# Kernel optimization log

Measured on AMD Instinct MI355X. Metric: run time of the kernel, lower is better.

## Reference

```python
import jax, jax.numpy as jnp
import numpy as np

D_MODEL = 512
HIDDEN = 2 * D_MODEL
B, L = 8, 2048
R_MIN, R_MAX = 0.8, 0.99
LN_EPS = 1e-5


def setup_inputs() -> dict:
    key = jax.random.key(0)
    ks = jax.random.split(key, 12)
    x = jax.random.normal(ks[0], (B, L, D_MODEL), jnp.float32)
    mask = jnp.ones((B, L), jnp.float32)
    # LRU eigenvalue init, exactly as the torch __init__
    u1 = jax.random.uniform(ks[1], (HIDDEN,), jnp.float32)
    u2 = jax.random.uniform(ks[2], (HIDDEN,), jnp.float32)
    nu_log = jnp.log(-0.5 * jnp.log(u1 * (R_MAX ** 2 - R_MIN ** 2) + R_MIN ** 2))
    theta_log = jnp.log(u2 * 2.0 * np.pi)
    diag_lambda = jnp.exp(jax.lax.complex(-jnp.exp(nu_log), jnp.exp(theta_log)))
    gamma_log = jnp.log(jnp.sqrt(1.0 - jnp.abs(diag_lambda) ** 2))
    params_log = jnp.stack([nu_log, theta_log, gamma_log])  # (3, HIDDEN)
    s_in = 1.0 / np.sqrt(D_MODEL)
    s_out = 1.0 / np.sqrt(HIDDEN)
    # complex Linear weights (real+imag parts; trained weights are fully complex)
    W_in_re = jax.random.uniform(ks[3], (HIDDEN, D_MODEL), jnp.float32, -s_in, s_in)
    W_in_im = jax.random.uniform(ks[4], (HIDDEN, D_MODEL), jnp.float32, -s_in, s_in)
    b_in_re = jax.random.uniform(ks[5], (HIDDEN,), jnp.float32, -s_in, s_in)
    b_in_im = jax.random.uniform(ks[6], (HIDDEN,), jnp.float32, -s_in, s_in)
    W_out_re = jax.random.uniform(ks[7], (D_MODEL, HIDDEN), jnp.float32, -s_out, s_out)
    W_out_im = jax.random.uniform(ks[8], (D_MODEL, HIDDEN), jnp.float32, -s_out, s_out)
    b_out_re = jax.random.uniform(ks[9], (D_MODEL,), jnp.float32, -s_out, s_out)
    b_out_im = jax.random.uniform(ks[10], (D_MODEL,), jnp.float32, -s_out, s_out)
    ln_w = jnp.ones((D_MODEL,), jnp.float32)
    ln_b = jnp.zeros((D_MODEL,), jnp.float32)
    return dict(x=x, mask=mask, params_log=params_log,
                W_in_re=W_in_re, W_in_im=W_in_im, b_in_re=b_in_re, b_in_im=b_in_im,
                W_out_re=W_out_re, W_out_im=W_out_im, b_out_re=b_out_re, b_out_im=b_out_im,
                ln_w=ln_w, ln_b=ln_b)


def _lru_parallel_scan(h, lamb, mask, Bn, Ln, Dn):
    # log-depth doubling trick over complex diagonal recurrence (faithful port)
    log2_L = int(np.ceil(np.log2(Ln)))
    for i in range(1, log2_L + 1):
        l = 2 ** i
        h = h.reshape(Bn * Ln // l, l, Dn)
        m = mask.reshape(Bn * Ln // l, l)
        h1, h2 = h[:, : l // 2], h[:, l // 2 :]
        if i > 1:
            lamb = jnp.concatenate([lamb, lamb * lamb[-1]], axis=0)  # powers lam^1..lam^(l/2)
        h2 = h2 + lamb * h1[:, -1:] * m[:, l // 2 - 1 : l // 2, None]
        h = jnp.concatenate([h1, h2], axis=1)
    return h.reshape(Bn, Ln, Dn)


def reference(x, mask, params_log, W_in_re, W_in_im, b_in_re, b_in_im,
              W_out_re, W_out_im, b_out_re, b_out_im, ln_w, ln_b):
    nu, theta, gamma = jnp.exp(params_log)  # each (HIDDEN,)
    lamb = jnp.exp(jax.lax.complex(-nu, theta))[None, :]  # (1, HIDDEN)
    W_in = jax.lax.complex(W_in_re, W_in_im)
    b_in = jax.lax.complex(b_in_re, b_in_im)
    W_out = jax.lax.complex(W_out_re, W_out_im)
    b_out = jax.lax.complex(b_out_re, b_out_im)
    xc = x.astype(jnp.complex64)
    h = (jnp.einsum('bld,hd->blh', xc, W_in) + b_in) * gamma  # (B, L, HIDDEN) complex64
    Bn, Ln, Dn = h.shape
    h = _lru_parallel_scan(h, lamb, mask, Bn, Ln, Dn)
    y = (jnp.einsum('blh,dh->bld', h, W_out) + b_out).real + x  # dropout = identity (eval)
    mean = jnp.mean(y, axis=-1, keepdims=True)
    var = jnp.var(y, axis=-1, keepdims=True)
    return (y - mean) / jnp.sqrt(var + LN_EPS) * ln_w + ln_b
```

## Files before the change

### kernel.cpp

```cpp
#include <hip/hip_runtime.h>
#include <hip/hip_bf16.h>
#include <cstdint>
#include <cstddef>


typedef unsigned short u16;
typedef __attribute__((ext_vector_type(8))) short bf16x8;
typedef __attribute__((ext_vector_type(4))) float f32x4;

#define B_    8
#define L_    2048
#define D_    512
#define H_    1024
#define M_    (B_ * L_)
#define SEG_  64
#define T_    (L_ / SEG_)

__device__ __forceinline__ float b2f(u16 u) {
  union { unsigned int i; float f; } v; v.i = ((unsigned int)u) << 16; return v.f;
}
__device__ __forceinline__ u16 f2b(float f) {
  union { float f; unsigned int i; } v; v.f = f;
  unsigned int x = v.i;
  return (u16)((x + 0x7fffu + ((x >> 16) & 1u)) >> 16);
}

__device__ __forceinline__ void gl2lds16(const void* g, void* l) {
  __builtin_amdgcn_global_load_lds(
      (const __attribute__((address_space(1))) void*)g,
      (__attribute__((address_space(3))) void*)l, 16, 0, 0);
}

__device__ __forceinline__ int ksw8(int row, int c) {
  return (c ^ (row & 7)) & 7;
}

__global__ __launch_bounds__(256) void prep_all(
    const float* __restrict__ x, u16* __restrict__ xb,
    const float* __restrict__ wire, const float* __restrict__ wiim,
    const float* __restrict__ wore, const float* __restrict__ woim,
    const float* __restrict__ bire, const float* __restrict__ biim,
    const float* __restrict__ params,
    u16* __restrict__ winb, u16* __restrict__ wcat, float* __restrict__ bb)
{
  int i = blockIdx.x * 256 + threadIdx.x;
#pragma unroll
  for (int j = 0; j < 4; ++j) {
    int gi = i + j * 524288;
    float4 v = ((const float4*)x)[gi];
    ushort4 o;
    o.x = f2b(v.x); o.y = f2b(v.y); o.z = f2b(v.z); o.w = f2b(v.w);
    ((ushort4*)xb)[gi] = o;
  }
  {
    int cp = i >> 9, k = i & 511;
    float g = expf(params[2 * H_ + cp]);
    winb[(size_t)(2 * cp) * 512 + k]     = f2b(wire[i] * g);
    winb[(size_t)(2 * cp + 1) * 512 + k] = f2b(wiim[i] * g);
  }
  {
    int d = i >> 10, c = i & 1023;
    wcat[(size_t)d * 2048 + 2 * c]     = f2b(wore[i]);
    wcat[(size_t)d * 2048 + 2 * c + 1] = f2b(-woim[i]);
  }
  if (i < 1024) {
    float gb = expf(params[2 * H_ + i]);
    bb[2 * i]     = bire[i] * gb;
    bb[2 * i + 1] = biim[i] * gb;
  }
}

__global__ __launch_bounds__(256, 4) void gemm_scan(
    const u16* __restrict__ A, const u16* __restrict__ Bp,
    const float* __restrict__ mask, const float* __restrict__ params,
    u16* __restrict__ h, const float* __restrict__ bb,
    float2* __restrict__ segfin, float* __restrict__ prodm)
{
  __shared__ __align__(16) u16 sAB[16384];
  __shared__ float mf[128];
  const int K = 512;

  const int tid  = threadIdx.x;
  const int lane = tid & 63;
  const int wave = tid >> 6;
  const int wm = wave >> 1, wn = wave & 1;
  const int m0 = blockIdx.x * 128;
  const int n0 = blockIdx.y * 128;
  const int b  = m0 >> 11;
  const int local0 = m0 & (L_ - 1);

  f32x4 acc[4][4];
#pragma unroll
  for (int i = 0; i < 4; ++i)
#pragma unroll
    for (int j = 0; j < 4; ++j) { f32x4 z = {0.f, 0.f, 0.f, 0.f}; acc[i][j] = z; }

  const int q = lane >> 4;
  const int r = lane & 15;

  for (int k0 = 0; k0 < K; k0 += 64) {
#pragma unroll
    for (int it = 0; it < 4; ++it) {
      int ci  = it * 256 + tid;
      int row = ci >> 3;
      int kc  = ksw8(row, ci & 7);
      gl2lds16(A  + (size_t)(m0 + row) * K + k0 + kc * 8, &sAB[ci * 8]);
      gl2lds16(Bp + (size_t)(n0 + row) * K + k0 + kc * 8, &sAB[8192 + ci * 8]);
    }
    __syncthreads();
#pragma unroll
    for (int kk = 0; kk < 2; ++kk) {
      const int cs = kk * 4 + q;
      bf16x8 af[4], bfv[4];
#pragma unroll
      for (int mt = 0; mt < 4; ++mt) {
        int arow = wm * 64 + mt * 16 + r;
        af[mt] = *(const bf16x8*)&sAB[(arow * 8 + ksw8(arow, cs)) * 8];
      }
#pragma unroll
      for (int nt = 0; nt < 4; ++nt) {
        int brow = wn * 64 + nt * 16 + r;
        bfv[nt] = *(const bf16x8*)&sAB[8192 + (brow * 8 + ksw8(brow, cs)) * 8];
      }
#pragma unroll
      for (int mt = 0; mt < 4; ++mt)
#pragma unroll
        for (int nt = 0; nt < 4; ++nt)
          acc[mt][nt] = __builtin_amdgcn_mfma_f32_16x16x32_bf16(
              bfv[nt], af[mt], acc[mt][nt], 0, 0, 0);
    }
    __syncthreads();
  }

  u16* sH = sAB;
  if (tid < 128)
    mf[tid] = (local0 + tid == 0) ? 0.f
                                  : mask[b * L_ + local0 + tid - 1];
#pragma unroll
  for (int mt = 0; mt < 4; ++mt) {
    const int trow = wm * 64 + mt * 16 + r;
    const int sw = (trow & 7) << 4;
#pragma unroll
    for (int nt = 0; nt < 4; ++nt) {
      const int nc = wn * 64 + nt * 16 + q * 4;
      const float4 b4 = *(const float4*)&bb[n0 + nc];
      ushort4 o;
      o.x = f2b(acc[mt][nt][0] + b4.x);
      o.y = f2b(acc[mt][nt][1] + b4.y);
      o.z = f2b(acc[mt][nt][2] + b4.z);
      o.w = f2b(acc[mt][nt][3] + b4.w);
      *(ushort4*)&sH[trow * 128 + (nc ^ sw)] = o;
    }
  }
  __syncthreads();

#pragma unroll
  for (int it = 0; it < 8; ++it) {
    int flat = it * 256 + tid;
    int row  = flat >> 4;
    int c16  = (flat & 15) * 8;
    bf16x8 v = *(const bf16x8*)&sH[row * 128 + (c16 ^ ((row & 7) << 4))];
    *(bf16x8*)&h[(size_t)(m0 + row) * 2048 + n0 + c16] = v;
  }

  {
    const int sIdx = wave;
    const int cpG  = (n0 >> 1) + lane;
    float nu = expf(params[cpG]);
    float th = expf(params[H_ + cpG]);
    float mg = expf(-nu);
    float lr = mg * cosf(th), li = mg * sinf(th);
    float sr = 0.f, si = 0.f, pm = 1.f;
    const int rbase = sIdx * 32;
#pragma unroll
    for (int t = 0; t < 32; ++t) {
      int row = rbase + t;
      int pos = row * 128 + ((lane * 2) ^ ((row & 7) << 4));
      ushort2 v = *(const ushort2*)&sH[pos];
      float fac = mf[row];
      pm *= fac;
      float nr = b2f(v.x) + fac * (lr * sr - li * si);
      float ni = b2f(v.y) + fac * (lr * si + li * sr);
      sr = nr; si = ni;
    }
    const int sG = (local0 >> 5) + sIdx;
    segfin[(size_t)(b * SEG_ + sG) * H_ + cpG] = make_float2(sr, si);
    if (lane == 0 && n0 == 0) prodm[b * SEG_ + sG] = pm;
  }
}

__global__ __launch_bounds__(256) void scan_carry(
    const float2* __restrict__ segfin, const float* __restrict__ prodm,
    const float* __restrict__ params, float2* __restrict__ carries)
{
  int idx = blockIdx.x * 256 + threadIdx.x;
  int b = idx >> 10, cp = idx & 1023;
  float nu = expf(params[cp]);
  float th = expf(params[H_ + cp]);
  float mg = expf(-nu);
  float ltr = mg * cosf(th), lti = mg * sinf(th);
#pragma unroll
  for (int sq = 0; sq < 5; ++sq) {
    float nr = ltr * ltr - lti * lti;
    float ni = 2.f * ltr * lti;
    ltr = nr; lti = ni;
  }
  float cr = 0.f, ci = 0.f;
  float2 fin = segfin[(size_t)(b * SEG_) * H_ + cp];
  float pmv = prodm[b * SEG_];
  for (int s = 0; s < SEG_; ++s) {
    size_t o = (size_t)(b * SEG_ + s) * H_ + cp;
    carries[o] = make_float2(cr, ci);
    float2 finn; float pmn;
    if (s + 1 < SEG_) { finn = segfin[o + H_]; pmn = prodm[b * SEG_ + s + 1]; }
    float nr = fin.x + pmv * (ltr * cr - lti * ci);
    float ni = fin.y + pmv * (ltr * ci + lti * cr);
    cr = nr; ci = ni;
    fin = finn; pmv = pmn;
  }
}

__global__ __launch_bounds__(256) void scan_full(
    u16* __restrict__ h, const float* __restrict__ mask,
    const float* __restrict__ params, const float2* __restrict__ carries)
{
  const int s = blockIdx.x, b = blockIdx.y;
  const int pa = threadIdx.x * 4;
  float lr[4], li[4], sr[4], si[4];
#pragma unroll
  for (int j = 0; j < 4; ++j) {
    int cp = pa + j;
    float nu = expf(params[cp]);
    float th = expf(params[H_ + cp]);
    float mg = expf(-nu);
    lr[j] = mg * cosf(th);
    li[j] = mg * sinf(th);
    float2 cv = carries[(size_t)(b * SEG_ + s) * H_ + cp];
    sr[j] = cv.x; si[j] = cv.y;
  }
  const int t0 = s * T_;
  u16* p = h + (size_t)(b * L_ + t0) * 2048 + pa * 2;
  const float* mp = mask + b * L_ + t0;
  float fac0;
  if (t0 == 0) fac0 = 0.f; else fac0 = mask[b * L_ + t0 - 1];

  bf16x8 buf[2][8];
#pragma unroll
  for (int j = 0; j < 8; ++j)
    buf[0][j] = *(const bf16x8*)(p + (size_t)j * 2048);
#pragma unroll
  for (int ch = 0; ch < T_ / 8; ++ch) {
    const int cur = ch & 1, nxt = cur ^ 1;
    if (ch < T_ / 8 - 1) {
      u16* pn = p + (size_t)(ch + 1) * 8 * 2048;
#pragma unroll
      for (int j = 0; j < 8; ++j)
        buf[nxt][j] = *(const bf16x8*)(pn + (size_t)j * 2048);
    }
#pragma unroll
    for (int j = 0; j < 8; ++j) {
      int i = ch * 8 + j;
      float fac = (i == 0) ? fac0 : mp[i - 1];
      u16 vv[8], ov[8];
      *(bf16x8*)vv = buf[cur][j];
#pragma unroll
      for (int k = 0; k < 4; ++k) {
        float ar = fac * sr[k], ai = fac * si[k];
        float nr = b2f(vv[2 * k])     + lr[k] * ar - li[k] * ai;
        float ni = b2f(vv[2 * k + 1]) + lr[k] * ai + li[k] * ar;
        sr[k] = nr; si[k] = ni;
        ov[2 * k]     = f2b(nr);
        ov[2 * k + 1] = f2b(ni);
      }
      *(bf16x8*)(p + (size_t)i * 2048) = *(bf16x8*)ov;
    }
  }
}

__global__ __launch_bounds__(512, 2) void gemm2_ln(
    const u16* __restrict__ A, const u16* __restrict__ Bp,
    const float* __restrict__ xg, const float* __restrict__ p0,
    const float* __restrict__ lnw, const float* __restrict__ lnb,
    float* __restrict__ out)
{
  __shared__ __align__(16) u16 smem[2][36864];

  const int K = 2048;
  const int tid  = threadIdx.x;
  const int lane = tid & 63;
  const int wave = tid >> 6;
  const int m0 = blockIdx.x * 64;
  const int q = lane >> 4;
  const int r = lane & 15;

  f32x4 acc[4][4];
#pragma unroll
  for (int i = 0; i < 4; ++i)
#pragma unroll
    for (int j = 0; j < 4; ++j) { f32x4 z = {0.f, 0.f, 0.f, 0.f}; acc[i][j] = z; }

  auto stage = [&](int bsel, int k0) {
    u16* sA = &smem[bsel][0];
    u16* sB = &smem[bsel][4096];
    {
      int ci  = tid;
      int row = ci >> 3;
      int kc  = ksw8(row, ci & 7);
      gl2lds16(A + (size_t)(m0 + row) * K + k0 + kc * 8, sA + ci * 8);
    }
#pragma unroll
    for (int it = 0; it < 8; ++it) {
      int ci  = it * 512 + tid;
      int row = ci >> 3;
      int kc  = ksw8(row, ci & 7);
      gl2lds16(Bp + (size_t)row * K + k0 + kc * 8, sB + ci * 8);
    }
  };

#define WAIT_VM9  asm volatile("s_waitcnt vmcnt(9)"  ::: "memory"); \
                  __builtin_amdgcn_sched_barrier(0)
#define WAIT_VM0  asm volatile("s_waitcnt vmcnt(0)"  ::: "memory"); \
                  __builtin_amdgcn_sched_barrier(0)
#define WAIT_LGKM asm volatile("s_waitcnt lgkmcnt(0)" ::: "memory"); \
                  __builtin_amdgcn_sched_barrier(0)
#define BAR()     __builtin_amdgcn_s_barrier(); \
                  __builtin_amdgcn_sched_barrier(0)

  stage(0, 0);
  stage(1, 64);
  WAIT_VM9;
  BAR();

  for (int t = 0; t < 32; ++t) {
    const int c = t & 1;
    const u16* sA = &smem[c][0];
    const u16* sB = &smem[c][4096];

    bf16x8 af[2][4], bfv[2][4];
#pragma unroll
    for (int kk = 0; kk < 2; ++kk) {
      const int cs = kk * 4 + q;
#pragma unroll
      for (int mt = 0; mt < 4; ++mt) {
        int arow = mt * 16 + r;
        af[kk][mt] = *(const bf16x8*)&sA[(arow * 8 + ksw8(arow, cs)) * 8];
      }
#pragma unroll
      for (int nt = 0; nt < 4; ++nt) {
        int brow = wave * 64 + nt * 16 + r;
        bfv[kk][nt] = *(const bf16x8*)&sB[(brow * 8 + ksw8(brow, cs)) * 8];
      }
    }
    WAIT_LGKM;
    BAR();

    if (t < 30) stage(c, (t + 2) * 64);
    __builtin_amdgcn_sched_barrier(0);

#pragma unroll
    for (int kk = 0; kk < 2; ++kk)
#pragma unroll
      for (int mt = 0; mt < 4; ++mt)
#pragma unroll
        for (int nt = 0; nt < 4; ++nt)
          acc[mt][nt] = __builtin_amdgcn_mfma_f32_16x16x32_bf16(
              bfv[kk][nt], af[kk][mt], acc[mt][nt], 0, 0, 0);

    if (t < 30)      { WAIT_VM9; }
    else if (t == 30){ WAIT_VM0; }
    if (t < 31)      { BAR(); }
  }

#undef WAIT_VM9
#undef WAIT_VM0
#undef WAIT_LGKM
#undef BAR

  __syncthreads();
  float* red_s  = (float*)&smem[0][0];
  float* red_ss = red_s + 512;

  float s[4] = {0.f, 0.f, 0.f, 0.f}, ss[4] = {0.f, 0.f, 0.f, 0.f};
#pragma unroll
  for (int mt = 0; mt < 4; ++mt) {
    const size_t grow = (size_t)(m0 + mt * 16 + r);
#pragma unroll
    for (int nt = 0; nt < 4; ++nt) {
      const int c4 = wave * 64 + nt * 16 + q * 4;
      const float4 b4 = *(const float4*)&p0[c4];
      const float4 x4 = *(const float4*)&xg[grow * 512 + c4];
      acc[mt][nt][0] += b4.x + x4.x;
      acc[mt][nt][1] += b4.y + x4.y;
      acc[mt][nt][2] += b4.z + x4.z;
      acc[mt][nt][3] += b4.w + x4.w;
#pragma unroll
      for (int j = 0; j < 4; ++j) {
        float z = acc[mt][nt][j];
        s[mt] += z; ss[mt] += z * z;
      }
    }
  }
#pragma unroll
  for (int mt = 0; mt < 4; ++mt) {
    s[mt]  += __shfl_xor(s[mt], 16);  s[mt]  += __shfl_xor(s[mt], 32);
    ss[mt] += __shfl_xor(ss[mt], 16); ss[mt] += __shfl_xor(ss[mt], 32);
  }
  if (q == 0) {
#pragma unroll
    for (int mt = 0; mt < 4; ++mt) {
      const int lr_ = mt * 16 + r;
      red_s[wave * 64 + lr_]  = s[mt];
      red_ss[wave * 64 + lr_] = ss[mt];
    }
  }
  __syncthreads();
#pragma unroll
  for (int mt = 0; mt < 4; ++mt) {
    const int lr_ = mt * 16 + r;
    float S = 0.f, SS = 0.f;
#pragma unroll
    for (int w = 0; w < 8; ++w) {
      S  += red_s[w * 64 + lr_];
      SS += red_ss[w * 64 + lr_];
    }
    const float mean = S * (1.f / 512.f);
    const float var  = SS * (1.f / 512.f) - mean * mean;
    const float inv  = rsqrtf(var + 1e-5f);
    const size_t grow = (size_t)(m0 + lr_);
#pragma unroll
    for (int nt = 0; nt < 4; ++nt) {
      const int c4 = wave * 64 + nt * 16 + q * 4;
      const float4 w4 = *(const float4*)&lnw[c4];
      const float4 g4 = *(const float4*)&lnb[c4];
      float4 o;
      o.x = (acc[mt][nt][0] - mean) * inv * w4.x + g4.x;
      o.y = (acc[mt][nt][1] - mean) * inv * w4.y + g4.y;
      o.z = (acc[mt][nt][2] - mean) * inv * w4.z + g4.z;
      o.w = (acc[mt][nt][3] - mean) * inv * w4.w + g4.w;
      *(float4*)&out[grow * 512 + c4] = o;
    }
  }
}

extern "C" void kernel_launch(void* const* d_in, const int* in_sizes, int n_in,
                              void* d_out, int out_size, void* d_ws, size_t ws_size,
                              hipStream_t stream) {
  (void)in_sizes; (void)n_in; (void)out_size; (void)ws_size;
  const float* x      = (const float*)d_in[0];
  const float* mask   = (const float*)d_in[1];
  const float* params = (const float*)d_in[2];
  const float* Wire   = (const float*)d_in[3];
  const float* Wiim   = (const float*)d_in[4];
  const float* bire   = (const float*)d_in[5];
  const float* biim   = (const float*)d_in[6];
  const float* Wore   = (const float*)d_in[7];
  const float* Woim   = (const float*)d_in[8];
  const float* bore   = (const float*)d_in[9];
  const float* lnw    = (const float*)d_in[11];
  const float* lnb    = (const float*)d_in[12];

  char* ws = (char*)d_ws;
  u16*    xb      = (u16*)   (ws);
  float2* segfin  = (float2*)(ws + (size_t)16777216);
  float2* carries = (float2*)(ws + (size_t)20971520);
  float*  prodm   = (float*) (ws + (size_t)25165824);
  u16*    h       = (u16*)   (ws + (size_t)33554432);
  u16*    winb    = (u16*)   (ws + (size_t)100663296);
  u16*    wcat    = (u16*)   (ws + (size_t)102760448);
  float*  bb      = (float*) (ws + (size_t)104857600);

  prep_all<<<2048, 256, 0, stream>>>(x, xb, Wire, Wiim, Wore, Woim,
                                     bire, biim, params, winb, wcat, bb);

  gemm_scan<<<dim3(128, 16), 256, 0, stream>>>(
      xb, winb, mask, params, h, bb, segfin, prodm);

  scan_carry<<<32, 256, 0, stream>>>(segfin, prodm, params, carries);
  scan_full<<<dim3(SEG_, B_), 256, 0, stream>>>(h, mask, params, carries);

  gemm2_ln<<<256, 512, 0, stream>>>(h, wcat, x, bore, lnw, lnb, (float*)d_out);
}
```

Before: 238.7 us.

## Load GEMM2 B operand directly into registers, stage only A through LDS

The second GEMM with fused LayerNorm no longer copies the weight (B) tiles into shared memory. Each wave now loads its B fragments straight from global memory into double-buffered registers, while only the A tile stays double-buffered in LDS. This removes the LDS write/read traffic for B and shrinks LDS use, and the loop is unrolled by two to alternate register buffers. In exchange it adds many VGPRs (launch bounds lowered to one block per SIMD group) and uses strided global loads for B that may coalesce poorly and depend on L2 hits.

```diff
diff --git a/kernel.cpp b/kernel.cpp
--- a/kernel.cpp
+++ b/kernel.cpp
@@ -277,13 +277,14 @@
   }
 }
 
-__global__ __launch_bounds__(512, 2) void gemm2_ln(
+__global__ __launch_bounds__(512, 1) void gemm2_ln(
     const u16* __restrict__ A, const u16* __restrict__ Bp,
     const float* __restrict__ xg, const float* __restrict__ p0,
     const float* __restrict__ lnw, const float* __restrict__ lnb,
     float* __restrict__ out)
 {
-  __shared__ __align__(16) u16 smem[2][36864];
+  __shared__ __align__(16) u16 sAbuf[2][4096];
+  __shared__ float red_s[512], red_ss[512];
 
   const int K = 2048;
   const int tid  = threadIdx.x;
@@ -293,28 +294,29 @@
   const int q = lane >> 4;
   const int r = lane & 15;
 
+  const u16* Aw = A + (size_t)m0 * K;
+
   f32x4 acc[4][4];
 #pragma unroll
   for (int i = 0; i < 4; ++i)
 #pragma unroll
     for (int j = 0; j < 4; ++j) { f32x4 z = {0.f, 0.f, 0.f, 0.f}; acc[i][j] = z; }
 
-  auto stage = [&](int bsel, int k0) {
-    u16* sA = &smem[bsel][0];
-    u16* sB = &smem[bsel][4096];
-    {
-      int ci  = tid;
-      int row = ci >> 3;
-      int kc  = ksw8(row, ci & 7);
-      gl2lds16(A + (size_t)(m0 + row) * K + k0 + kc * 8, sA + ci * 8);
-    }
-#pragma unroll
-    for (int it = 0; it < 8; ++it) {
-      int ci  = it * 512 + tid;
-      int row = ci >> 3;
-      int kc  = ksw8(row, ci & 7);
-      gl2lds16(Bp + (size_t)row * K + k0 + kc * 8, sB + ci * 8);
-    }
+  auto stage_a = [&](int bsel, int k0) {
+    int ci  = tid;
+    int row = ci >> 3;
+    int kc  = ksw8(row, ci & 7);
+    gl2lds16(Aw + (size_t)row * K + k0 + kc * 8, &sAbuf[bsel][ci * 8]);
+  };
+  auto load_b = [&](bf16x8 (&bv)[8], int k0) {
+#pragma unroll
+    for (int kk = 0; kk < 2; ++kk)
+#pragma unroll
+      for (int nt = 0; nt < 4; ++nt) {
+        int brow = wave * 64 + nt * 16 + r;
+        bv[kk * 4 + nt] = *(const bf16x8*)&Bp[(size_t)brow * K + k0
+                                              + (kk * 4 + q) * 8];
+      }
   };
 
 #define WAIT_VM9  asm volatile("s_waitcnt vmcnt(9)"  ::: "memory"); \
@@ -326,37 +328,33 @@
 #define BAR()     __builtin_amdgcn_s_barrier(); \
                   __builtin_amdgcn_sched_barrier(0)
 
-  stage(0, 0);
-  stage(1, 64);
+  bf16x8 bva[8], bvb[8];
+
+  stage_a(0, 0);
+  __builtin_amdgcn_sched_barrier(0);
+  load_b(bva, 0);
+  __builtin_amdgcn_sched_barrier(0);
+  stage_a(1, 64);
+  __builtin_amdgcn_sched_barrier(0);
+  load_b(bvb, 64);
+  __builtin_amdgcn_sched_barrier(0);
   WAIT_VM9;
   BAR();
 
-  for (int t = 0; t < 32; ++t) {
-    const int c = t & 1;
-    const u16* sA = &smem[c][0];
-    const u16* sB = &smem[c][4096];
-
-    bf16x8 af[2][4], bfv[2][4];
-#pragma unroll
-    for (int kk = 0; kk < 2; ++kk) {
-      const int cs = kk * 4 + q;
+  auto step = [&](const u16* sA, u16* sAw, bf16x8 (&bv)[8], int t) {
+    bf16x8 af[8];
+#pragma unroll
+    for (int kk = 0; kk < 2; ++kk)
 #pragma unroll
       for (int mt = 0; mt < 4; ++mt) {
         int arow = mt * 16 + r;
-        af[kk][mt] = *(const bf16x8*)&sA[(arow * 8 + ksw8(arow, cs)) * 8];
-      }
-#pragma unroll
-      for (int nt = 0; nt < 4; ++nt) {
-        int brow = wave * 64 + nt * 16 + r;
-        bfv[kk][nt] = *(const bf16x8*)&sB[(brow * 8 + ksw8(brow, cs)) * 8];
-      }
-    }
+        af[kk * 4 + mt] =
+            *(const bf16x8*)&sA[(arow * 8 + ksw8(arow, kk * 4 + q)) * 8];
+      }
     WAIT_LGKM;
     BAR();
-
-    if (t < 30) stage(c, (t + 2) * 64);
+    if (t < 30) stage_a(t & 1, (t + 2) * 64);
     __builtin_amdgcn_sched_barrier(0);
-
 #pragma unroll
     for (int kk = 0; kk < 2; ++kk)
 #pragma unroll
@@ -364,21 +362,26 @@
 #pragma unroll
         for (int nt = 0; nt < 4; ++nt)
           acc[mt][nt] = __builtin_amdgcn_mfma_f32_16x16x32_bf16(
-              bfv[kk][nt], af[kk][mt], acc[mt][nt], 0, 0, 0);
-
-    if (t < 30)      { WAIT_VM9; }
-    else if (t == 30){ WAIT_VM0; }
-    if (t < 31)      { BAR(); }
+              bv[kk * 4 + nt], af[kk * 4 + mt], acc[mt][nt], 0, 0, 0);
+    if (t < 30) load_b(bv, (t + 2) * 64);
+    __builtin_amdgcn_sched_barrier(0);
+    if (t < 30)       { WAIT_VM9; }
+    else if (t == 30) { WAIT_VM0; }
+    if (t < 31)       { BAR(); }
+    (void)sAw;
+  };
+
+#pragma unroll 1
+  for (int tt = 0; tt < 16; ++tt) {
+    const int t = tt * 2;
+    step(&sAbuf[0][0], &sAbuf[0][0], bva, t);
+    step(&sAbuf[1][0], &sAbuf[1][0], bvb, t + 1);
   }
 
 #undef WAIT_VM9
 #undef WAIT_VM0
 #undef WAIT_LGKM
 #undef BAR
-
-  __syncthreads();
-  float* red_s  = (float*)&smem[0][0];
-  float* red_ss = red_s + 512;
 
   float s[4] = {0.f, 0.f, 0.f, 0.f}, ss[4] = {0.f, 0.f, 0.f, 0.f};
 #pragma unroll
```

Result: slower. 267.5 us (+12.0%).

## Fuse final scan pass into output GEMM prologue on LDS tiles

Applied to the files above, without the earlier changes.

Removes the separate scan_full kernel. The second GEMM now applies the intra-segment carry recurrence directly to the A tile after it lands in LDS, before the MFMA fragments are read. Lambda values are precomputed once into a table in the prep kernel. This avoids a full read-modify-write pass over the large h buffer. The cost is a serial 32-step scan done by one wave per K-tile, plus an extra barrier each iteration, inside the GEMM's main loop. Occupancy hint drops to 1 block per SM.

```diff
diff --git a/kernel.cpp b/kernel.cpp
--- a/kernel.cpp
+++ b/kernel.cpp
@@ -41,7 +41,8 @@
     const float* __restrict__ wore, const float* __restrict__ woim,
     const float* __restrict__ bire, const float* __restrict__ biim,
     const float* __restrict__ params,
-    u16* __restrict__ winb, u16* __restrict__ wcat, float* __restrict__ bb)
+    u16* __restrict__ winb, u16* __restrict__ wcat, float* __restrict__ bb,
+    float2* __restrict__ lamtab)
 {
   int i = blockIdx.x * 256 + threadIdx.x;
 #pragma unroll
@@ -67,6 +68,10 @@
     float gb = expf(params[2 * H_ + i]);
     bb[2 * i]     = bire[i] * gb;
     bb[2 * i + 1] = biim[i] * gb;
+    float nu = expf(params[i]);
+    float th = expf(params[H_ + i]);
+    float mg = expf(-nu);
+    lamtab[i] = make_float2(mg * cosf(th), mg * sinf(th));
   }
 }
 
@@ -220,76 +225,25 @@
   }
 }
 
-__global__ __launch_bounds__(256) void scan_full(
-    u16* __restrict__ h, const float* __restrict__ mask,
-    const float* __restrict__ params, const float2* __restrict__ carries)
-{
-  const int s = blockIdx.x, b = blockIdx.y;
-  const int pa = threadIdx.x * 4;
-  float lr[4], li[4], sr[4], si[4];
-#pragma unroll
-  for (int j = 0; j < 4; ++j) {
-    int cp = pa + j;
-    float nu = expf(params[cp]);
-    float th = expf(params[H_ + cp]);
-    float mg = expf(-nu);
-    lr[j] = mg * cosf(th);
-    li[j] = mg * sinf(th);
-    float2 cv = carries[(size_t)(b * SEG_ + s) * H_ + cp];
-    sr[j] = cv.x; si[j] = cv.y;
-  }
-  const int t0 = s * T_;
-  u16* p = h + (size_t)(b * L_ + t0) * 2048 + pa * 2;
-  const float* mp = mask + b * L_ + t0;
-  float fac0;
-  if (t0 == 0) fac0 = 0.f; else fac0 = mask[b * L_ + t0 - 1];
-
-  bf16x8 buf[2][8];
-#pragma unroll
-  for (int j = 0; j < 8; ++j)
-    buf[0][j] = *(const bf16x8*)(p + (size_t)j * 2048);
-#pragma unroll
-  for (int ch = 0; ch < T_ / 8; ++ch) {
-    const int cur = ch & 1, nxt = cur ^ 1;
-    if (ch < T_ / 8 - 1) {
-      u16* pn = p + (size_t)(ch + 1) * 8 * 2048;
-#pragma unroll
-      for (int j = 0; j < 8; ++j)
-        buf[nxt][j] = *(const bf16x8*)(pn + (size_t)j * 2048);
-    }
-#pragma unroll
-    for (int j = 0; j < 8; ++j) {
-      int i = ch * 8 + j;
-      float fac = (i == 0) ? fac0 : mp[i - 1];
-      u16 vv[8], ov[8];
-      *(bf16x8*)vv = buf[cur][j];
-#pragma unroll
-      for (int k = 0; k < 4; ++k) {
-        float ar = fac * sr[k], ai = fac * si[k];
-        float nr = b2f(vv[2 * k])     + lr[k] * ar - li[k] * ai;
-        float ni = b2f(vv[2 * k + 1]) + lr[k] * ai + li[k] * ar;
-        sr[k] = nr; si[k] = ni;
-        ov[2 * k]     = f2b(nr);
-        ov[2 * k + 1] = f2b(ni);
-      }
-      *(bf16x8*)(p + (size_t)i * 2048) = *(bf16x8*)ov;
-    }
-  }
-}
-
-__global__ __launch_bounds__(512, 2) void gemm2_ln(
+__global__ __launch_bounds__(512, 1) void gemm2_ln(
     const u16* __restrict__ A, const u16* __restrict__ Bp,
     const float* __restrict__ xg, const float* __restrict__ p0,
     const float* __restrict__ lnw, const float* __restrict__ lnb,
-    float* __restrict__ out)
+    const float* __restrict__ mask, const float2* __restrict__ lamtab,
+    const float2* __restrict__ carries, float* __restrict__ out)
 {
   __shared__ __align__(16) u16 smem[2][36864];
+  __shared__ float mf_s[64];
+  __shared__ float red_s[512], red_ss[512];
 
   const int K = 2048;
   const int tid  = threadIdx.x;
   const int lane = tid & 63;
   const int wave = tid >> 6;
   const int m0 = blockIdx.x * 64;
+  const int b  = m0 >> 11;
+  const int local0 = m0 & (L_ - 1);
+  const int s0 = local0 >> 5;
   const int q = lane >> 4;
   const int r = lane & 15;
 
@@ -317,6 +271,14 @@
     }
   };
 
+  const int sp = lane & 31;
+  const int sg = lane >> 5;
+  const int schunk = sp >> 2;
+  const int soff = (sp & 3) * 4;
+
+  float lrA = 0.f, liA = 0.f, crA = 0.f, ciA = 0.f;
+  float lrB = 0.f, liB = 0.f, crB = 0.f, ciB = 0.f;
+
 #define WAIT_VM9  asm volatile("s_waitcnt vmcnt(9)"  ::: "memory"); \
                   __builtin_amdgcn_sched_barrier(0)
 #define WAIT_VM0  asm volatile("s_waitcnt vmcnt(0)"  ::: "memory"); \
@@ -326,15 +288,47 @@
 #define BAR()     __builtin_amdgcn_s_barrier(); \
                   __builtin_amdgcn_sched_barrier(0)
 
+  if (tid < 64) {
+    int gr = local0 + tid;
+    mf_s[tid] = (gr == 0) ? 0.f : mask[b * L_ + gr - 1];
+  }
+  if (wave == 0) {
+    int cp = sp;
+    float2 lv = lamtab[cp];
+    float2 cv = carries[((size_t)(b * SEG_) + s0 + sg) * H_ + cp];
+    lrA = lv.x; liA = lv.y; crA = cv.x; ciA = cv.y;
+  }
+  __builtin_amdgcn_sched_barrier(0);
   stage(0, 0);
   stage(1, 64);
   WAIT_VM9;
   BAR();
 
-  for (int t = 0; t < 32; ++t) {
+  auto step = [&](int t, float lrS, float liS, float crS, float ciS,
+                  float& lrN, float& liN, float& crN, float& ciN) {
     const int c = t & 1;
-    const u16* sA = &smem[c][0];
+    u16* sA = &smem[c][0];
     const u16* sB = &smem[c][4096];
+
+    if (wave == 0) {
+      float sr = crS, si = ciS;
+      char* base = (char*)sA;
+#pragma unroll
+      for (int i = 0; i < 32; ++i) {
+        int row = sg * 32 + i;
+        float fac = mf_s[row];
+        int addr = row * 128 + (((schunk ^ (row & 7)) & 7) << 4) + soff;
+        unsigned int v = *(unsigned int*)(base + addr);
+        float ar = fac * sr, ai = fac * si;
+        float nr = b2f((u16)(v & 0xffffu))  + lrS * ar - liS * ai;
+        float ni = b2f((u16)(v >> 16))      + lrS * ai + liS * ar;
+        sr = nr; si = ni;
+        unsigned int ov = (unsigned int)f2b(nr) | ((unsigned int)f2b(ni) << 16);
+        *(unsigned int*)(base + addr) = ov;
+      }
+      WAIT_LGKM;
+    }
+    BAR();
 
     bf16x8 af[2][4], bfv[2][4];
 #pragma unroll
@@ -354,6 +348,13 @@
     WAIT_LGKM;
     BAR();
 
+    if (wave == 0 && t < 31) {
+      int cp = (t + 1) * 32 + sp;
+      float2 lv = lamtab[cp];
+      float2 cv = carries[((size_t)(b * SEG_) + s0 + sg) * H_ + cp];
+      lrN = lv.x; liN = lv.y; crN = cv.x; ciN = cv.y;
+    }
+    __builtin_amdgcn_sched_barrier(0);
     if (t < 30) stage(c, (t + 2) * 64);
     __builtin_amdgcn_sched_barrier(0);
 
@@ -366,19 +367,21 @@
           acc[mt][nt] = __builtin_amdgcn_mfma_f32_16x16x32_bf16(
               bfv[kk][nt], af[kk][mt], acc[mt][nt], 0, 0, 0);
 
-    if (t < 30)      { WAIT_VM9; }
-    else if (t == 30){ WAIT_VM0; }
-    if (t < 31)      { BAR(); }
+    if (t < 30)       { WAIT_VM9; }
+    else if (t == 30) { WAIT_VM0; }
+    if (t < 31)       { BAR(); }
+  };
+
+#pragma unroll 1
+  for (int tt = 0; tt < 16; ++tt) {
+    step(tt * 2,     lrA, liA, crA, ciA, lrB, liB, crB, ciB);
+    step(tt * 2 + 1, lrB, liB, crB, ciB, lrA, liA, crA, ciA);
   }
 
 #undef WAIT_VM9
 #undef WAIT_VM0
 #undef WAIT_LGKM
 #undef BAR
-
-  __syncthreads();
-  float* red_s  = (float*)&smem[0][0];
-  float* red_ss = red_s + 512;
 
   float s[4] = {0.f, 0.f, 0.f, 0.f}, ss[4] = {0.f, 0.f, 0.f, 0.f};
 #pragma unroll
@@ -464,19 +467,20 @@
   float2* segfin  = (float2*)(ws + (size_t)16777216);
   float2* carries = (float2*)(ws + (size_t)20971520);
   float*  prodm   = (float*) (ws + (size_t)25165824);
+  float2* lamtab  = (float2*)(ws + (size_t)26214400);
   u16*    h       = (u16*)   (ws + (size_t)33554432);
   u16*    winb    = (u16*)   (ws + (size_t)100663296);
   u16*    wcat    = (u16*)   (ws + (size_t)102760448);
   float*  bb      = (float*) (ws + (size_t)104857600);
 
   prep_all<<<2048, 256, 0, stream>>>(x, xb, Wire, Wiim, Wore, Woim,
-                                     bire, biim, params, winb, wcat, bb);
+                                     bire, biim, params, winb, wcat, bb, lamtab);
 
   gemm_scan<<<dim3(128, 16), 256, 0, stream>>>(
       xb, winb, mask, params, h, bb, segfin, prodm);
 
   scan_carry<<<32, 256, 0, stream>>>(segfin, prodm, params, carries);
-  scan_full<<<dim3(SEG_, B_), 256, 0, stream>>>(h, mask, params, carries);
-
-  gemm2_ln<<<256, 512, 0, stream>>>(h, wcat, x, bore, lnw, lnb, (float*)d_out);
-}
+
+  gemm2_ln<<<256, 512, 0, stream>>>(h, wcat, x, bore, lnw, lnb,
+                                    mask, lamtab, carries, (float*)d_out);
+}
```

Result: slower. 308.2 us (+29.1%).
